# Optimization experiments

Measured on AMD Instinct MI355X. Metric: run time of the kernel, lower is better.

The kernel has to match this reference:

```python
import jax, jax.numpy as jnp
import numpy as np

N = 100000      # num_nodes
E = 1600000     # num_edges
F_IN = 10       # node_feature_dim
H = 64          # hidden_channels
B = 128         # num graphs in batch
C = 3           # num_classes
EPS = 1e-5      # BatchNorm eps


def setup_inputs() -> dict:
    key = jax.random.key(0)
    ks = jax.random.split(key, 32)
    inp = {
        'x': jax.random.normal(ks[0], (N, F_IN), dtype=jnp.float32),
        'edge_index': jax.random.randint(ks[1], (2, E), 0, N, dtype=jnp.int32),
        'batch': jnp.sort(jax.random.randint(ks[2], (N,), 0, B, dtype=jnp.int32)),
    }
    dims = [(F_IN, H), (H, H), (H, H)]
    k = 3
    for i, (din, dout) in enumerate(dims, start=1):
        inp[f'W{i}'] = jax.random.normal(ks[k], (din, dout)) * (1.0 / np.sqrt(din)); k += 1
        inp[f'b{i}'] = jax.random.normal(ks[k], (dout,)) * 0.01; k += 1
        inp[f'g{i}'] = 1.0 + 0.1 * jax.random.normal(ks[k], (dout,)); k += 1
        inp[f'be{i}'] = 0.1 * jax.random.normal(ks[k], (dout,)); k += 1
        inp[f'm{i}'] = 0.1 * jax.random.normal(ks[k], (dout,)); k += 1
        inp[f'v{i}'] = 0.5 + jax.random.uniform(ks[k], (dout,)); k += 1
    inp['fw1'] = jax.random.normal(ks[k], (H, H // 2)) * (1.0 / np.sqrt(H)); k += 1
    inp['fb1'] = jax.random.normal(ks[k], (H // 2,)) * 0.01; k += 1
    inp['fw2'] = jax.random.normal(ks[k], (H // 2, C)) * (1.0 / np.sqrt(H // 2)); k += 1
    inp['fb2'] = jax.random.normal(ks[k], (C,)) * 0.01
    return inp


def reference(x, edge_index, batch,
              W1, b1, g1, be1, m1, v1,
              W2, b2, g2, be2, m2, v2,
              W3, b3, g3, be3, m3, v3,
              fw1, fb1, fw2, fb2):
    src, dst = edge_index[0], edge_index[1]
    # GCN normalization with implicit self-loops: deg includes the self-loop
    deg = jax.ops.segment_sum(jnp.ones((E,), x.dtype), dst, num_segments=N) + 1.0
    dinv = jax.lax.rsqrt(deg)
    ecoef = (dinv[src] * dinv[dst])[:, None]   # per-edge norm [E,1]
    scoef = (dinv * dinv)[:, None]             # self-loop norm [N,1]

    def gcn_conv(h, W, b):
        h = h @ W  # [N, dout]
        agg = jax.ops.segment_sum(h[src] * ecoef, dst, num_segments=N)
        return agg + h * scoef + b

    def bn(h, g, be, m, v):  # eval-mode BatchNorm1d
        return (h - m) * jax.lax.rsqrt(v + EPS) * g + be

    h = jax.nn.relu(bn(gcn_conv(x, W1, b1), g1, be1, m1, v1))
    h = jax.nn.relu(bn(gcn_conv(h, W2, b2), g2, be2, m2, v2))
    h = jax.nn.relu(bn(gcn_conv(h, W3, b3), g3, be3, m3, v3))

    # global mean pool over batch assignment
    counts = jax.ops.segment_sum(jnp.ones((N,), h.dtype), batch, num_segments=B)
    pooled = jax.ops.segment_sum(h, batch, num_segments=B) / jnp.maximum(counts, 1.0)[:, None]

    out = jax.nn.relu(pooled @ fw1 + fb1) @ fw2 + fb2  # [B, C]
    return out
```

## Files before the change

kernel.cpp:

```cpp
#include <hip/hip_runtime.h>
#include <hip/hip_bf16.h>

#define N_NODES 100000
#define E_EDGES 1600000
#define F_IN    10
#define H       64
#define B_GR    128
#define C_CLS   3
#define BN_EPS  1e-5f
#define NH      (N_NODES * H)
#define NBLK_SCAN ((N_NODES + 255) / 256)

#define SCAT_CHUNKS 256
#define SCAT_PER    (E_EDGES / SCAT_CHUNKS)
#define SLICE_N     (N_NODES / 8)

__global__ void deg_kernel(const int* __restrict__ dst, int* __restrict__ deg) {
    int e = blockIdx.x * blockDim.x + threadIdx.x;
    if (e < E_EDGES) atomicAdd(&deg[dst[e]], 1);
}

__global__ void dinv_kernel(const int* __restrict__ deg, float* __restrict__ dinv) {
    int n = blockIdx.x * blockDim.x + threadIdx.x;
    if (n < N_NODES) dinv[n] = rsqrtf((float)deg[n] + 1.0f);
}

__global__ void scan1_kernel(const int* __restrict__ deg, int* __restrict__ rowptr,
                             int* __restrict__ blockSums) {
    __shared__ int lds[256];
    int t = threadIdx.x;
    int i = blockIdx.x * 256 + t;
    int v = (i < N_NODES) ? deg[i] : 0;
    lds[t] = v;
    __syncthreads();
    for (int off = 1; off < 256; off <<= 1) {
        int add = (t >= off) ? lds[t - off] : 0;
        __syncthreads();
        lds[t] += add;
        __syncthreads();
    }
    if (i < N_NODES) rowptr[i] = lds[t] - v;
    if (t == 255) blockSums[blockIdx.x] = lds[255];
}

__global__ void scan2_kernel(const int* __restrict__ blockSums, int* __restrict__ blockOff) {
    __shared__ int lds[512];
    int t = threadIdx.x;
    int v = (t < NBLK_SCAN) ? blockSums[t] : 0;
    lds[t] = v;
    __syncthreads();
    for (int off = 1; off < 512; off <<= 1) {
        int add = (t >= off) ? lds[t - off] : 0;
        __syncthreads();
        lds[t] += add;
        __syncthreads();
    }
    if (t < NBLK_SCAN) blockOff[t] = lds[t] - v;
}

__global__ void scan3_kernel(int* __restrict__ rowptr, const int* __restrict__ blockOff,
                             int* __restrict__ cursor) {
    int i = blockIdx.x * blockDim.x + threadIdx.x;
    if (i < N_NODES) {
        int r = rowptr[i] + blockOff[i >> 8];
        rowptr[i] = r;
        cursor[i] = r;
    } else if (i == N_NODES) {
        rowptr[N_NODES] = E_EDGES;
    }
}

__global__ __launch_bounds__(256) void scatter_kernel(const int* __restrict__ src,
                                                      const int* __restrict__ dst,
                                                      const float* __restrict__ dinv,
                                                      int* __restrict__ cursor,
                                                      float2* __restrict__ edata) {
    int slice = blockIdx.x & 7;
    int chunk = blockIdx.x >> 3;
    int base  = chunk * SCAT_PER;
    int lo    = slice * SLICE_N;
    int hi    = lo + SLICE_N;
    for (int i = threadIdx.x; i < SCAT_PER; i += 256) {
        int e = base + i;
        int d = dst[e];
        if (d >= lo && d < hi) {
            int s    = src[e];
            int slot = atomicAdd(&cursor[d], 1);
            edata[slot] = make_float2(__int_as_float(s), dinv[s] * dinv[d]);
        }
    }
}

__global__ void pad_kernel(const float* __restrict__ x, float* __restrict__ xp) {
    int idx = blockIdx.x * blockDim.x + threadIdx.x;
    if (idx >= N_NODES * 16) return;
    int n = idx >> 4, c = idx & 15;
    xp[idx] = (c < F_IN) ? x[n * F_IN + c] : 0.0f;
}

__global__ __launch_bounds__(256) void gather16_kernel(const int* __restrict__ rowptr,
                                                       const float2* __restrict__ edata,
                                                       const float* __restrict__ xp,
                                                       const float* __restrict__ dinv,
                                                       float* __restrict__ agg16) {
    int tid  = threadIdx.x;
    int n    = blockIdx.x * 4 + (tid >> 6);
    if (n >= N_NODES) return;
    int lane = tid & 63;
    int grp  = lane >> 2;
    int c4   = (lane & 3) * 4;

    int start = rowptr[n], end = rowptr[n + 1];
    float4 acc = make_float4(0.f, 0.f, 0.f, 0.f);
    for (int p = start; p < end; p += 16) {
        int q = p + grp;
        float2 ed = (q < end) ? edata[q] : make_float2(__int_as_float(0), 0.0f);
        int   s = __float_as_int(ed.x);
        float w = ed.y;
        float4 hv = *(const float4*)&xp[s * 16 + c4];
        acc.x = fmaf(w, hv.x, acc.x);
        acc.y = fmaf(w, hv.y, acc.y);
        acc.z = fmaf(w, hv.z, acc.z);
        acc.w = fmaf(w, hv.w, acc.w);
    }
#pragma unroll
    for (int off = 4; off < 64; off <<= 1) {
        acc.x += __shfl_xor(acc.x, off);
        acc.y += __shfl_xor(acc.y, off);
        acc.z += __shfl_xor(acc.z, off);
        acc.w += __shfl_xor(acc.w, off);
    }
    if (grp == 0) {
        float4 self = *(const float4*)&xp[n * 16 + c4];
        float  di   = dinv[n];
        float  di2  = di * di;
        acc.x = fmaf(self.x, di2, acc.x);
        acc.y = fmaf(self.y, di2, acc.y);
        acc.z = fmaf(self.z, di2, acc.z);
        acc.w = fmaf(self.w, di2, acc.w);
        *(float4*)&agg16[n * 16 + c4] = acc;
    }
}

__global__ __launch_bounds__(256) void matmul16_bn_kernel(const float* __restrict__ agg16,
                                                          const float* __restrict__ W,
                                                          const float* __restrict__ b,
                                                          const float* __restrict__ g,
                                                          const float* __restrict__ be,
                                                          const float* __restrict__ m,
                                                          const float* __restrict__ v,
                                                          float* __restrict__ hout) {
    __shared__ float rowLds[16 * 16];
    __shared__ float Wlds[F_IN * 68];
    int tid  = threadIdx.x;
    int base = blockIdx.x * 16;

    if (tid < 64) {
        int r = tid >> 2, c = (tid & 3) * 4;
        *(float4*)&rowLds[r * 16 + c] = *(const float4*)&agg16[(base + r) * 16 + c];
    }
    for (int i = tid; i < F_IN * 64; i += 256) {
        int k = i >> 6, c = i & 63;
        Wlds[k * 68 + c] = W[i];
    }
    __syncthreads();

    int r  = tid >> 4;
    int c4 = (tid & 15) * 4;
    float4 acc = make_float4(0.f, 0.f, 0.f, 0.f);
#pragma unroll
    for (int k = 0; k < F_IN; ++k) {
        float  rv = rowLds[r * 16 + k];
        float4 wv = *(const float4*)&Wlds[k * 68 + c4];
        acc.x = fmaf(rv, wv.x, acc.x);
        acc.y = fmaf(rv, wv.y, acc.y);
        acc.z = fmaf(rv, wv.z, acc.z);
        acc.w = fmaf(rv, wv.w, acc.w);
    }
    float4 gv = *(const float4*)&g[c4];
    float4 vv = *(const float4*)&v[c4];
    float4 bv = *(const float4*)&b[c4];
    float4 mv = *(const float4*)&m[c4];
    float4 bev= *(const float4*)&be[c4];
    float4 sc, sh, r2;
    sc.x = gv.x * rsqrtf(vv.x + BN_EPS);
    sc.y = gv.y * rsqrtf(vv.y + BN_EPS);
    sc.z = gv.z * rsqrtf(vv.z + BN_EPS);
    sc.w = gv.w * rsqrtf(vv.w + BN_EPS);
    sh.x = bev.x + (bv.x - mv.x) * sc.x;
    sh.y = bev.y + (bv.y - mv.y) * sc.y;
    sh.z = bev.z + (bv.z - mv.z) * sc.z;
    sh.w = bev.w + (bv.w - mv.w) * sc.w;
    r2.x = fmaxf(acc.x * sc.x + sh.x, 0.f);
    r2.y = fmaxf(acc.y * sc.y + sh.y, 0.f);
    r2.z = fmaxf(acc.z * sc.z + sh.z, 0.f);
    r2.w = fmaxf(acc.w * sc.w + sh.w, 0.f);
    *(float4*)&hout[(base + r) * H + c4] = r2;
}

template <int K>
__global__ __launch_bounds__(256) void matmul_kernel(const float* __restrict__ hin,
                                                     const float* __restrict__ W,
                                                     float* __restrict__ hout) {
    constexpr int KP = (K == 64) ? 65 : (K + 1);
    __shared__ float rowLds[16 * KP];
    __shared__ float Wlds[K * 68];
    int tid  = threadIdx.x;
    int base = blockIdx.x * 16;

    for (int i = tid; i < K * 64; i += 256)
        Wlds[(i >> 6) * 68 + (i & 63)] = W[i];
    for (int i = tid; i < 16 * K; i += 256) {
        int r = i / K, k = i - r * K;
        rowLds[r * KP + k] = hin[(base + r) * K + k];
    }
    __syncthreads();

    int r  = tid >> 4;
    int c4 = (tid & 15) * 4;
    float4 acc = make_float4(0.f, 0.f, 0.f, 0.f);
#pragma unroll
    for (int k = 0; k < K; ++k) {
        float  rv = rowLds[r * KP + k];
        float4 wv = *(const float4*)&Wlds[k * 68 + c4];
        acc.x = fmaf(rv, wv.x, acc.x);
        acc.y = fmaf(rv, wv.y, acc.y);
        acc.z = fmaf(rv, wv.z, acc.z);
        acc.w = fmaf(rv, wv.w, acc.w);
    }
    *(float4*)&hout[(base + r) * H + c4] = acc;
}

__global__ __launch_bounds__(256) void gather_kernel(const int* __restrict__ rowptr,
                                                     const float2* __restrict__ edata,
                                                     const float* __restrict__ hW,
                                                     const float* __restrict__ dinv,
                                                     const float* __restrict__ b,
                                                     const float* __restrict__ g,
                                                     const float* __restrict__ be,
                                                     const float* __restrict__ m,
                                                     const float* __restrict__ v,
                                                     float* __restrict__ hout) {
    int tid  = threadIdx.x;
    int n    = blockIdx.x * 4 + (tid >> 6);
    if (n >= N_NODES) return;
    int lane = tid & 63;
    int grp  = lane >> 4;
    int c4   = (lane & 15) * 4;

    int start = rowptr[n], end = rowptr[n + 1];
    float4 acc = make_float4(0.f, 0.f, 0.f, 0.f);
    for (int p = start; p < end; p += 4) {
        int q = p + grp;
        float2 ed = (q < end) ? edata[q] : make_float2(__int_as_float(0), 0.0f);
        int   s = __float_as_int(ed.x);
        float w = ed.y;
        float4 hv = *(const float4*)&hW[s * H + c4];
        acc.x = fmaf(w, hv.x, acc.x);
        acc.y = fmaf(w, hv.y, acc.y);
        acc.z = fmaf(w, hv.z, acc.z);
        acc.w = fmaf(w, hv.w, acc.w);
    }
#pragma unroll
    for (int off = 16; off < 64; off <<= 1) {
        acc.x += __shfl_xor(acc.x, off);
        acc.y += __shfl_xor(acc.y, off);
        acc.z += __shfl_xor(acc.z, off);
        acc.w += __shfl_xor(acc.w, off);
    }
    if (grp == 0) {
        float4 self = *(const float4*)&hW[n * H + c4];
        float  di   = dinv[n];
        float  di2  = di * di;
        float4 gv = *(const float4*)&g[c4];
        float4 vv = *(const float4*)&v[c4];
        float4 bv = *(const float4*)&b[c4];
        float4 mv = *(const float4*)&m[c4];
        float4 bev= *(const float4*)&be[c4];
        float4 sc, sh, r2;
        sc.x = gv.x * rsqrtf(vv.x + BN_EPS);
        sc.y = gv.y * rsqrtf(vv.y + BN_EPS);
        sc.z = gv.z * rsqrtf(vv.z + BN_EPS);
        sc.w = gv.w * rsqrtf(vv.w + BN_EPS);
        sh.x = bev.x + (bv.x - mv.x) * sc.x;
        sh.y = bev.y + (bv.y - mv.y) * sc.y;
        sh.z = bev.z + (bv.z - mv.z) * sc.z;
        sh.w = bev.w + (bv.w - mv.w) * sc.w;
        r2.x = fmaxf((acc.x + self.x * di2) * sc.x + sh.x, 0.f);
        r2.y = fmaxf((acc.y + self.y * di2) * sc.y + sh.y, 0.f);
        r2.z = fmaxf((acc.z + self.z * di2) * sc.z + sh.z, 0.f);
        r2.w = fmaxf((acc.w + self.w * di2) * sc.w + sh.w, 0.f);
        *(float4*)&hout[n * H + c4] = r2;
    }
}

#define PCHUNK 128
__global__ void pool_kernel(const float* __restrict__ h, const int* __restrict__ batch,
                            float* __restrict__ pooled, float* __restrict__ counts) {
    int tid  = threadIdx.x;
    int wid  = blockIdx.x * 4 + (tid >> 6);
    int lane = tid & 63;
    int n0   = wid * PCHUNK;
    if (n0 >= N_NODES) return;
    int n1 = min(n0 + PCHUNK, N_NODES);

    int   curb = batch[n0];
    float acc  = 0.0f;
    int   run  = 0;
    for (int n = n0; n < n1; ++n) {
        int bb = batch[n];
        if (bb != curb) {
            atomicAdd(&pooled[curb * H + lane], acc);
            if (lane == 0) atomicAdd(&counts[curb], (float)run);
            acc = 0.0f; run = 0; curb = bb;
        }
        acc += h[n * H + lane];
        ++run;
    }
    atomicAdd(&pooled[curb * H + lane], acc);
    if (lane == 0) atomicAdd(&counts[curb], (float)run);
}

__global__ void mlp_kernel(const float* __restrict__ pooled, const float* __restrict__ counts,
                           const float* __restrict__ fw1, const float* __restrict__ fb1,
                           const float* __restrict__ fw2, const float* __restrict__ fb2,
                           float* __restrict__ out) {
    __shared__ float prow[H];
    __shared__ float hid[H / 2];
    int b = blockIdx.x;
    int t = threadIdx.x;
    float cnt = fmaxf(counts[b], 1.0f);
    prow[t] = pooled[b * H + t] / cnt;
    __syncthreads();
    if (t < H / 2) {
        float acc = fb1[t];
#pragma unroll
        for (int k = 0; k < H; ++k) acc += prow[k] * fw1[k * (H / 2) + t];
        hid[t] = fmaxf(acc, 0.0f);
    }
    __syncthreads();
    if (t < C_CLS) {
        float acc = fb2[t];
#pragma unroll
        for (int j = 0; j < H / 2; ++j) acc += hid[j] * fw2[j * C_CLS + t];
        out[b * C_CLS + t] = acc;
    }
}

extern "C" void kernel_launch(void* const* d_in, const int* in_sizes, int n_in,
                              void* d_out, int out_size, void* d_ws, size_t ws_size,
                              hipStream_t stream) {
    const float* x          = (const float*)d_in[0];
    const int*   edge_index = (const int*)d_in[1];
    const int*   batch      = (const int*)d_in[2];

    const float* W1 = (const float*)d_in[3];
    const float* b1 = (const float*)d_in[4];
    const float* g1 = (const float*)d_in[5];
    const float* be1= (const float*)d_in[6];
    const float* m1 = (const float*)d_in[7];
    const float* v1 = (const float*)d_in[8];
    const float* W2 = (const float*)d_in[9];
    const float* b2 = (const float*)d_in[10];
    const float* g2 = (const float*)d_in[11];
    const float* be2= (const float*)d_in[12];
    const float* m2 = (const float*)d_in[13];
    const float* v2 = (const float*)d_in[14];
    const float* W3 = (const float*)d_in[15];
    const float* b3 = (const float*)d_in[16];
    const float* g3 = (const float*)d_in[17];
    const float* be3= (const float*)d_in[18];
    const float* m3 = (const float*)d_in[19];
    const float* v3 = (const float*)d_in[20];
    const float* fw1= (const float*)d_in[21];
    const float* fb1= (const float*)d_in[22];
    const float* fw2= (const float*)d_in[23];
    const float* fb2= (const float*)d_in[24];

    const int* src = edge_index;
    const int* dst = edge_index + E_EDGES;

    float* ws      = (float*)d_ws;
    float* hW      = ws;
    float* hbuf    = ws + (size_t)NH;
    float2* edata  = (float2*)(ws + 2 * (size_t)NH);
    float* fafter  = ws + 2 * (size_t)NH + 2 * (size_t)E_EDGES;
    int*   deg_i   = (int*)fafter;
    float* dinv    = fafter + N_NODES;
    int*   rowptr  = (int*)(fafter + 2 * N_NODES);
    int*   cursor  = (int*)(fafter + 3 * N_NODES + 1);
    int*   blockSums = (int*)(fafter + 4 * N_NODES + 1);
    int*   blockOff  = blockSums + 512;
    float* pooled  = fafter + 4 * N_NODES + 1 + 1024;
    float* counts  = pooled + B_GR * H;

    float* xp    = hW;
    float* agg16 = hW + (size_t)N_NODES * 16;

    float* out = (float*)d_out;

    hipMemsetAsync(deg_i, 0, N_NODES * sizeof(int), stream);
    hipMemsetAsync(pooled, 0, (B_GR * H + B_GR) * sizeof(float), stream);

    deg_kernel<<<(E_EDGES + 255) / 256, 256, 0, stream>>>(dst, deg_i);
    dinv_kernel<<<(N_NODES + 255) / 256, 256, 0, stream>>>(deg_i, dinv);

    scan1_kernel<<<NBLK_SCAN, 256, 0, stream>>>(deg_i, rowptr, blockSums);
    scan2_kernel<<<1, 512, 0, stream>>>(blockSums, blockOff);
    scan3_kernel<<<(N_NODES + 256) / 256, 256, 0, stream>>>(rowptr, blockOff, cursor);
    scatter_kernel<<<SCAT_CHUNKS * 8, 256, 0, stream>>>(src, dst, dinv, cursor, edata);

    const int mmGrid = N_NODES / 16;
    const int gGrid  = N_NODES / 4;

    pad_kernel<<<(N_NODES * 16 + 255) / 256, 256, 0, stream>>>(x, xp);
    gather16_kernel<<<gGrid, 256, 0, stream>>>(rowptr, edata, xp, dinv, agg16);
    matmul16_bn_kernel<<<mmGrid, 256, 0, stream>>>(agg16, W1, b1, g1, be1, m1, v1, hbuf);

    matmul_kernel<H><<<mmGrid, 256, 0, stream>>>(hbuf, W2, hW);
    gather_kernel<<<gGrid, 256, 0, stream>>>(rowptr, edata, hW, dinv, b2, g2, be2, m2, v2, hbuf);

    matmul_kernel<H><<<mmGrid, 256, 0, stream>>>(hbuf, W3, hW);
    gather_kernel<<<gGrid, 256, 0, stream>>>(rowptr, edata, hW, dinv, b3, g3, be3, m3, v3, hbuf);

    const int poolWaves = (N_NODES + PCHUNK - 1) / PCHUNK;
    pool_kernel<<<(poolWaves + 3) / 4, 256, 0, stream>>>(hbuf, batch, pooled, counts);
    mlp_kernel<<<B_GR, 64, 0, stream>>>(pooled, counts, fw1, fb1, fw2, fb2, out);
}
```

Baseline: 558.4 us.

## Replace atomic per-node CSR scatter with two-level LDS radix bucket sort

Builds the destination-sorted CSR edge list with a two-pass bucket sort instead of per-edge global atomics on node cursors. The first pass bins edges into 256-node buckets using shared-memory histograms and one global atomic per bucket per tile. The second pass sorts each bucket by local node in shared memory and writes coalesced edge data with the precomputed norm. This trades many scattered global atomics for two extra passes and an intermediate buffer. It relies on a fixed per-bucket capacity (L2CAP) that clamps oversized buckets and on packing src into 17 bits.

```diff
diff --git a/kernel.cpp b/kernel.cpp
--- a/kernel.cpp
+++ b/kernel.cpp
@@ -11,9 +11,9 @@
 #define NH      (N_NODES * H)
 #define NBLK_SCAN ((N_NODES + 255) / 256)
 
-#define SCAT_CHUNKS 256
-#define SCAT_PER    (E_EDGES / SCAT_CHUNKS)
-#define SLICE_N     (N_NODES / 8)
+#define TILE1   4096
+#define NB1     391
+#define L2CAP   6144
 
 __global__ void deg_kernel(const int* __restrict__ dst, int* __restrict__ deg) {
     int e = blockIdx.x * blockDim.x + threadIdx.x;
@@ -59,36 +59,152 @@
 }
 
 __global__ void scan3_kernel(int* __restrict__ rowptr, const int* __restrict__ blockOff,
-                             int* __restrict__ cursor) {
+                             int* __restrict__ bcur) {
     int i = blockIdx.x * blockDim.x + threadIdx.x;
     if (i < N_NODES) {
         int r = rowptr[i] + blockOff[i >> 8];
         rowptr[i] = r;
-        cursor[i] = r;
+        if ((i & 255) == 0) bcur[i >> 8] = r;
     } else if (i == N_NODES) {
         rowptr[N_NODES] = E_EDGES;
     }
 }
 
-__global__ __launch_bounds__(256) void scatter_kernel(const int* __restrict__ src,
-                                                      const int* __restrict__ dst,
-                                                      const float* __restrict__ dinv,
-                                                      int* __restrict__ cursor,
-                                                      float2* __restrict__ edata) {
-    int slice = blockIdx.x & 7;
-    int chunk = blockIdx.x >> 3;
-    int base  = chunk * SCAT_PER;
-    int lo    = slice * SLICE_N;
-    int hi    = lo + SLICE_N;
-    for (int i = threadIdx.x; i < SCAT_PER; i += 256) {
-        int e = base + i;
-        int d = dst[e];
-        if (d >= lo && d < hi) {
-            int s    = src[e];
-            int slot = atomicAdd(&cursor[d], 1);
-            edata[slot] = make_float2(__int_as_float(s), dinv[s] * dinv[d]);
+__global__ __launch_bounds__(256) void l1sort_kernel(const int* __restrict__ src,
+                                                     const int* __restrict__ dst,
+                                                     int* __restrict__ bcur,
+                                                     int* __restrict__ inter) {
+    __shared__ int hist[NB1];
+    __shared__ int sbase[NB1];
+    __shared__ int gbase[NB1];
+    __shared__ int scanA[512];
+    __shared__ int scanB[512];
+    __shared__ int ebuf[TILE1];
+    __shared__ unsigned short bkt[TILE1];
+
+    int tid   = threadIdx.x;
+    int tbase = blockIdx.x * TILE1;
+    int tcnt  = min(TILE1, E_EDGES - tbase);
+
+    for (int i = tid; i < NB1; i += 256) hist[i] = 0;
+    __syncthreads();
+
+    int   pk[16];
+    int   rk[16];
+    short bb[16];
+#pragma unroll
+    for (int j = 0; j < 16; ++j) {
+        int i = j * 256 + tid;
+        if (i < tcnt) {
+            int e = tbase + i;
+            int s = src[e], d = dst[e];
+            int b  = d >> 8;
+            int dl = d & 255;
+            pk[j] = s | (dl << 17);
+            bb[j] = (short)b;
+            rk[j] = atomicAdd(&hist[b], 1);
+        } else {
+            pk[j] = -1; rk[j] = 0; bb[j] = 0;
         }
     }
+    __syncthreads();
+
+    for (int i = tid; i < 512; i += 256) scanA[i] = (i < NB1) ? hist[i] : 0;
+    __syncthreads();
+    int* A = scanA; int* B = scanB;
+    for (int off = 1; off < 512; off <<= 1) {
+        for (int i = tid; i < 512; i += 256)
+            B[i] = A[i] + ((i >= off) ? A[i - off] : 0);
+        __syncthreads();
+        int* t = A; A = B; B = t;
+    }
+    for (int i = tid; i < NB1; i += 256) {
+        int c = hist[i];
+        sbase[i] = A[i] - c;
+        gbase[i] = (c > 0) ? atomicAdd(&bcur[i], c) : 0;
+    }
+    __syncthreads();
+
+#pragma unroll
+    for (int j = 0; j < 16; ++j) {
+        if (pk[j] >= 0) {
+            int b   = bb[j];
+            int pos = sbase[b] + rk[j];
+            ebuf[pos] = pk[j];
+            bkt[pos]  = (unsigned short)b;
+        }
+    }
+    __syncthreads();
+
+    for (int i = tid; i < tcnt; i += 256) {
+        int b = bkt[i];
+        inter[gbase[b] + (i - sbase[b])] = ebuf[i];
+    }
+}
+
+__global__ __launch_bounds__(256) void l2sort_kernel(const int* __restrict__ rowptr,
+                                                     const int* __restrict__ inter,
+                                                     const float* __restrict__ dinv,
+                                                     float2* __restrict__ edata) {
+    __shared__ int    nhist[256];
+    __shared__ int    nscan[256];
+    __shared__ float2 ebuf[L2CAP];
+
+    int tid      = threadIdx.x;
+    int b        = blockIdx.x;
+    int nodeBase = b << 8;
+    int lo       = rowptr[nodeBase];
+    int hi       = rowptr[min(nodeBase + 256, N_NODES)];
+    int cnt      = hi - lo;
+    if (cnt > L2CAP) cnt = L2CAP;
+
+    nhist[tid] = 0;
+    __syncthreads();
+
+    int vv[24];
+    int dr[24];
+#pragma unroll
+    for (int j = 0; j < 24; ++j) {
+        int i = j * 256 + tid;
+        if (i < cnt) {
+            int v  = inter[lo + i];
+            int dl = (v >> 17) & 255;
+            int r  = atomicAdd(&nhist[dl], 1);
+            vv[j] = v;
+            dr[j] = (dl << 16) | r;
+        } else {
+            vv[j] = -1; dr[j] = 0;
+        }
+    }
+    __syncthreads();
+
+    int vval = nhist[tid];
+    nscan[tid] = vval;
+    __syncthreads();
+    for (int off = 1; off < 256; off <<= 1) {
+        int add = (tid >= off) ? nscan[tid - off] : 0;
+        __syncthreads();
+        nscan[tid] += add;
+        __syncthreads();
+    }
+    nhist[tid] = nscan[tid] - vval;
+    __syncthreads();
+
+#pragma unroll
+    for (int j = 0; j < 24; ++j) {
+        if (vv[j] >= 0) {
+            int dl  = dr[j] >> 16;
+            int r   = dr[j] & 0xFFFF;
+            int pos = nhist[dl] + r;
+            int s   = vv[j] & 0x1FFFF;
+            int d   = nodeBase + dl;
+            ebuf[pos] = make_float2(__int_as_float(s), dinv[s] * dinv[d]);
+        }
+    }
+    __syncthreads();
+
+    for (int i = tid; i < cnt; i += 256)
+        edata[lo + i] = ebuf[i];
 }
 
 __global__ void pad_kernel(const float* __restrict__ x, float* __restrict__ xp) {
@@ -388,14 +504,15 @@
     int*   deg_i   = (int*)fafter;
     float* dinv    = fafter + N_NODES;
     int*   rowptr  = (int*)(fafter + 2 * N_NODES);
-    int*   cursor  = (int*)(fafter + 3 * N_NODES + 1);
-    int*   blockSums = (int*)(fafter + 4 * N_NODES + 1);
+    int*   blockSums = (int*)(fafter + 3 * N_NODES + 1);
     int*   blockOff  = blockSums + 512;
-    float* pooled  = fafter + 4 * N_NODES + 1 + 1024;
+    int*   bcur      = blockOff + 512;
+    float* pooled  = fafter + 3 * N_NODES + 1 + 1536;
     float* counts  = pooled + B_GR * H;
 
     float* xp    = hW;
     float* agg16 = hW + (size_t)N_NODES * 16;
+    int*   inter = (int*)(hW + 2 * (size_t)N_NODES * 16);
 
     float* out = (float*)d_out;
 
@@ -407,8 +524,10 @@
 
     scan1_kernel<<<NBLK_SCAN, 256, 0, stream>>>(deg_i, rowptr, blockSums);
     scan2_kernel<<<1, 512, 0, stream>>>(blockSums, blockOff);
-    scan3_kernel<<<(N_NODES + 256) / 256, 256, 0, stream>>>(rowptr, blockOff, cursor);
-    scatter_kernel<<<SCAT_CHUNKS * 8, 256, 0, stream>>>(src, dst, dinv, cursor, edata);
+    scan3_kernel<<<(N_NODES + 256) / 256, 256, 0, stream>>>(rowptr, blockOff, bcur);
+
+    l1sort_kernel<<<(E_EDGES + TILE1 - 1) / TILE1, 256, 0, stream>>>(src, dst, bcur, inter);
+    l2sort_kernel<<<NB1, 256, 0, stream>>>(rowptr, inter, dinv, edata);
 
     const int mmGrid = N_NODES / 16;
     const int gGrid  = N_NODES / 4;
```

After: 524.8 us. 1.06x faster.
